# Kernel optimization log

Hardware: AMD Instinct MI355X
Metric: run time of the kernel (lower is better)

## Reference

```python
import jax, jax.numpy as jnp
import numpy as np
from jax import lax

B, T, D, H, K = 8, 1024, 1024, 16, 3
DK = D // H


def setup_inputs() -> dict:
    key = jax.random.key(0)
    ks = jax.random.split(key, 12)
    s = 0.02
    queries = jax.random.normal(ks[0], (B, T, D), dtype=jnp.float32)
    keys = jax.random.normal(ks[1], (B, T, D), dtype=jnp.float32)
    values = jax.random.normal(ks[2], (B, T, D), dtype=jnp.float32)
    # causal mask: True = masked (strict upper triangle)
    attn_mask = jnp.triu(jnp.ones((T, T), dtype=bool), k=1)
    # key padding mask: last 128 keys padded for every batch element
    src_key_padding_mask = jnp.broadcast_to(jnp.arange(T) >= T - 128, (B, T))
    conv_q_w = jax.random.normal(ks[3], (D, D, K), dtype=jnp.float32) * s  # (out, in, k)
    conv_q_b = jax.random.normal(ks[4], (D,), dtype=jnp.float32) * s
    conv_k_w = jax.random.normal(ks[5], (D, D, K), dtype=jnp.float32) * s
    conv_k_b = jax.random.normal(ks[6], (D,), dtype=jnp.float32) * s
    v_w = jax.random.normal(ks[7], (D, D), dtype=jnp.float32) * s   # torch Linear weight [out,in]
    v_b = jax.random.normal(ks[8], (D,), dtype=jnp.float32) * s
    out_w = jax.random.normal(ks[9], (D, D), dtype=jnp.float32) * s
    out_b = jax.random.normal(ks[10], (D,), dtype=jnp.float32) * s
    return {"queries": queries, "keys": keys, "values": values,
            "attn_mask": attn_mask, "src_key_padding_mask": src_key_padding_mask,
            "conv_q_w": conv_q_w, "conv_q_b": conv_q_b,
            "conv_k_w": conv_k_w, "conv_k_b": conv_k_b,
            "v_w": v_w, "v_b": v_b, "out_w": out_w, "out_b": out_b}


def _conv1d_same(x, w, b):
    # x: [B, T, D] -> conv over time with 'same' padding (pad_l=(K-1)//2, pad_r=K//2)
    pad_l, pad_r = (K - 1) // 2, K // 2
    xc = jnp.pad(x.transpose(0, 2, 1), ((0, 0), (0, 0), (pad_l, pad_r)))  # [B, D, T+K-1]
    y = lax.conv_general_dilated(xc, w, window_strides=(1,), padding='VALID',
                                 dimension_numbers=('NCH', 'OIH', 'NCH'))  # [B, D, T]
    return y.transpose(0, 2, 1) + b  # [B, T, D]


def _attention(queries, keys, values, attn_mask, key_padding_mask,
               conv_q_w, conv_q_b, conv_k_w, conv_k_b, v_w, v_b, out_w, out_b):
    q_out = _conv1d_same(queries, conv_q_w, conv_q_b)  # [B, Tq, D]
    k_out = _conv1d_same(keys, conv_k_w, conv_k_b)     # [B, Tk, D]
    v_out = values @ v_w.T + v_b                        # [B, Tk, D]

    Q = q_out.reshape(B, T, H, DK).transpose(0, 2, 1, 3)  # [B, H, Tq, dk]
    Kh = k_out.reshape(B, T, H, DK).transpose(0, 2, 1, 3)
    V = v_out.reshape(B, T, H, DK).transpose(0, 2, 1, 3)

    scores = jnp.einsum('bhqd,bhkd->bhqk', Q, Kh) / jnp.sqrt(jnp.float32(DK))
    neg = jnp.float32(-jnp.inf)
    scores = jnp.where(key_padding_mask[:, None, None, :], neg, scores)
    scores = jnp.where(attn_mask[None, None, :, :], neg, scores)
    attn_weights = jax.nn.softmax(scores, axis=-1)  # dropout is identity at eval
    attn_output = jnp.einsum('bhqk,bhkd->bhqd', attn_weights, V)
    attn_output = attn_output.transpose(0, 2, 1, 3).reshape(B, T, D)
    return attn_output @ out_w.T + out_b, attn_weights


def reference(queries, keys, values, attn_mask, src_key_padding_mask,
              conv_q_w, conv_q_b, conv_k_w, conv_k_b, v_w, v_b, out_w, out_b):
    return _attention(queries, keys, values, attn_mask, src_key_padding_mask,
                      conv_q_w, conv_q_b, conv_k_w, conv_k_b, v_w, v_b, out_w, out_b)
```

## Files before the change

kernel.cpp:

```cpp
#include <hip/hip_runtime.h>

typedef unsigned short u16;
typedef unsigned int   u32;
typedef __bf16 bf16x8 __attribute__((ext_vector_type(8)));
typedef float  f32x4  __attribute__((ext_vector_type(4)));
typedef const __attribute__((address_space(1))) u32* gas1_t;
typedef __attribute__((address_space(3))) u32*       las3_t;

#define DEV static __device__ __forceinline__
#define MFMA16(a, b, c) __builtin_amdgcn_mfma_f32_16x16x32_bf16((a), (b), (c), 0, 0, 0)

DEV u16 f2b(float f) {
  u32 u = __builtin_bit_cast(u32, f);
  return (u16)((u + 0x7fffu + ((u >> 16) & 1u)) >> 16);
}
DEV float b2f(u16 h) { return __builtin_bit_cast(float, (u32)h << 16); }

DEV void stage16(const void* g, void* l) {
  __builtin_amdgcn_global_load_lds((gas1_t)g, (las3_t)l, 16, 0, 0);
}

DEV int rfl(int x) { return __builtin_amdgcn_readfirstlane(x); }

extern "C" __global__ __launch_bounds__(256)
void k_prep(const float* __restrict__ s0, const float* __restrict__ s1,
            const float* __restrict__ s2, const float* __restrict__ s3,
            const float* __restrict__ s4, const float* __restrict__ wq,
            const float* __restrict__ wk, u16* __restrict__ dqkv,
            u16* __restrict__ dvw, u16* __restrict__ dow,
            u16* __restrict__ wtbase, u16* __restrict__ zbuf) {
  __shared__ float ls[3072];
  const int y = blockIdx.y, tid = threadIdx.x;
  if (y < 5) {
    const float* src = y == 0 ? s0 : y == 1 ? s1 : y == 2 ? s2 : y == 3 ? s3 : s4;
    u16* dst = y < 3 ? dqkv + (size_t)y * 8388608 : (y == 3 ? dvw : dow);
    const int n4 = y < 3 ? 2097152 : 262144;
    int i = blockIdx.x * 256 + tid;
    int st = gridDim.x * 256;
    for (; i < n4; i += st) {
      float4 v = ((const float4*)src)[i];
      ushort4 o;
      o.x = f2b(v.x); o.y = f2b(v.y); o.z = f2b(v.z); o.w = f2b(v.w);
      ((ushort4*)dst)[i] = o;
    }
  } else if (y < 7) {
    const int o = blockIdx.x, zz = y - 5;
    const float* src = (zz ? wk : wq) + (size_t)o * 3072;
#pragma unroll
    for (int s = 0; s < 3; ++s)
      ((float4*)ls)[s * 256 + tid] = ((const float4*)src)[s * 256 + tid];
    __syncthreads();
    u16* dst = wtbase + (size_t)zz * 3145728 + (size_t)o * 3072;
#pragma unroll
    for (int s = 0; s < 12; ++s) {
      int j = s * 256 + tid;
      int k = j >> 10, ii = j & 1023;
      dst[j] = f2b(ls[ii * 3 + k]);
    }
  } else {
    if (blockIdx.x == 0) zbuf[tid] = 0;
  }
}

template <int FUSED3, int OUTF32>
__global__ __launch_bounds__(256)
void k_gemm(const u16* __restrict__ Abase, const u16* __restrict__ Btbase,
            const float* __restrict__ b0, const float* __restrict__ b1,
            const float* __restrict__ b2, void* __restrict__ Cbase,
            u16* __restrict__ vT, const u16* __restrict__ zbuf) {
  __shared__ __align__(16) u16 smem[17408];
  const int z = FUSED3 ? blockIdx.z : 0;
  const bool conv = FUSED3 && (z < 2);
  const int K = conv ? 3072 : 1024;
  const u16* A = Abase + (size_t)z * 8388608;
  const u16* Bt = Btbase + (size_t)z * 3145728;
  const float* bias = z == 0 ? b0 : z == 1 ? b1 : b2;
  const int tid = threadIdx.x, lane = tid & 63, wave = tid >> 6;
  const int wm = wave >> 1, wn = wave & 1;
  const int l15 = lane & 15, gr = lane >> 4;
  const int r0 = blockIdx.y * 128, n0 = blockIdx.x * 128;
  const int srow = tid >> 3, scol = (tid & 7) * 8;
  u16* sA = smem;
  f32x4 acc[4][4] = {};

  if (conv) {
    u16* sB = smem + 8320;
    const int bb = r0 >> 10;
    const int tb = (r0 & 1023) - 1;
#pragma unroll 1
    for (int t = 0; t < 16; ++t) {
      const int c0 = t * 64;
#pragma unroll
      for (int s = 0; s < 5; ++s) {
        const int e = s * 256 + tid;
        if (e < 1040) {
          const int lr = e >> 3, ch = (e & 7) * 8;
          const int tt = tb + lr;
          const u16* g = ((u32)tt < 1024u)
              ? (A + (((size_t)((bb << 10) + tt)) << 10) + c0 + ch)
              : (zbuf + ch);
          stage16(g, (char*)smem + rfl((s * 256 + wave * 64) * 16));
        }
      }
#pragma unroll
      for (int s3 = 0; s3 < 3; ++s3) {
#pragma unroll
        for (int s = 0; s < 4; ++s) {
          const int row = s * 32 + srow;
          stage16(Bt + (size_t)(n0 + row) * 3072 + s3 * 1024 + c0 + scol,
                  (char*)smem + rfl(16640 + (s * 256 + wave * 64) * 16));
        }
        __syncthreads();
#pragma unroll
        for (int ks = 0; ks < 2; ++ks) {
          bf16x8 af[4], bfr[4];
          const int koff = ks * 32 + gr * 8;
#pragma unroll
          for (int f = 0; f < 4; ++f)
            af[f] = *(const bf16x8*)&sA[(wm * 64 + f * 16 + l15 + s3) * 64 + koff];
#pragma unroll
          for (int f = 0; f < 4; ++f)
            bfr[f] = *(const bf16x8*)&sB[(wn * 64 + f * 16 + l15) * 64 + koff];
#pragma unroll
          for (int i = 0; i < 4; ++i)
#pragma unroll
            for (int j = 0; j < 4; ++j)
              acc[i][j] = MFMA16(af[i], bfr[j], acc[i][j]);
        }
        __syncthreads();
      }
    }
  } else {
    u16* sB = smem + 8192;
    const int nt = K >> 6;
    for (int t = 0; t < nt; ++t) {
      const int k0 = t * 64;
#pragma unroll
      for (int s = 0; s < 4; ++s) {
        const int row = s * 32 + srow;
        stage16(A + (size_t)(r0 + row) * K + k0 + scol,
                (char*)smem + rfl((s * 256 + wave * 64) * 16));
        stage16(Bt + (size_t)(n0 + row) * K + k0 + scol,
                (char*)smem + rfl(16384 + (s * 256 + wave * 64) * 16));
      }
      __syncthreads();
#pragma unroll
      for (int ks = 0; ks < 2; ++ks) {
        bf16x8 af[4], bfr[4];
        const int koff = ks * 32 + gr * 8;
#pragma unroll
        for (int f = 0; f < 4; ++f)
          af[f] = *(const bf16x8*)&sA[(wm * 64 + f * 16 + l15) * 64 + koff];
#pragma unroll
        for (int f = 0; f < 4; ++f)
          bfr[f] = *(const bf16x8*)&sB[(wn * 64 + f * 16 + l15) * 64 + koff];
#pragma unroll
        for (int i = 0; i < 4; ++i)
#pragma unroll
          for (int j = 0; j < 4; ++j)
            acc[i][j] = MFMA16(af[i], bfr[j], acc[i][j]);
      }
      __syncthreads();
    }
  }

  if (FUSED3 && z == 2) {
    u16* tp = smem;
#pragma unroll
    for (int i = 0; i < 4; ++i)
#pragma unroll
      for (int j = 0; j < 4; ++j) {
        const int cl = wn * 64 + j * 16 + l15;
        const float bv = bias[n0 + cl];
        const int rl0 = wm * 64 + i * 16 + gr * 4;
        union { u16 h[4]; ushort4 v4; } tv;
#pragma unroll
        for (int r = 0; r < 4; ++r) tv.h[r] = f2b(acc[i][j][r] + bv);
        *(ushort4*)&tp[cl * 136 + rl0] = tv.v4;
      }
    __syncthreads();
    const int bb2 = r0 >> 10, tof = r0 & 1023;
    const int drb = tid >> 4, ch16 = (tid & 15) * 8;
#pragma unroll
    for (int g = 0; g < 8; ++g) {
      const int dr = g * 16 + drb;
      uint4 v4 = *(const uint4*)&tp[dr * 136 + ch16];
      *(uint4*)&vT[(((size_t)((bb2 << 10) + n0 + dr)) << 10) + tof + ch16] = v4;
    }
  } else {
    void* Cout = OUTF32 ? Cbase : (void*)((u16*)Cbase + (size_t)z * 8388608);
#pragma unroll
    for (int i = 0; i < 4; ++i)
#pragma unroll
      for (int j = 0; j < 4; ++j) {
        const int colg = n0 + wn * 64 + j * 16 + l15;
        const float bv = bias[colg];
#pragma unroll
        for (int r = 0; r < 4; ++r) {
          const int rowg = r0 + wm * 64 + i * 16 + gr * 4 + r;
          float v = acc[i][j][r] + bv;
          if (OUTF32) ((float*)Cout)[(size_t)rowg * 1024 + colg] = v;
          else        ((u16*)Cout)[(size_t)rowg * 1024 + colg] = f2b(v);
        }
      }
  }
}

__global__ __launch_bounds__(256)
void k_attn(const u16* __restrict__ Qg, const u16* __restrict__ Kg,
            const u16* __restrict__ Vtg, float* __restrict__ Wout,
            u16* __restrict__ Og) {
  __shared__ __align__(16) u16 sQ[128 * 64];
  __shared__ __align__(16) u16 sK[64 * 64];
  __shared__ __align__(16) u16 sV[64 * 64];
  __shared__ __align__(16) u16 sP[4][32 * 64];
  const int tid = threadIdx.x, lane = tid & 63, wave = tid >> 6;
  const int q0 = blockIdx.x * 128, h = blockIdx.y, b = blockIdx.z;
  const u16* Qh = Qg + ((size_t)b * 1024) * 1024 + h * 64;
  const u16* Kh = Kg + ((size_t)b * 1024) * 1024 + h * 64;
  const u16* Vh = Vtg + (size_t)b * 1024 * 1024 + ((size_t)h * 64) * 1024;
  float* Wh = Wout + (((size_t)b * 16 + h) * 1024) * 1024;

#pragma unroll
  for (int s = 0; s < 4; ++s) {
    int e = s * 256 + tid;
    int row = e >> 3, col = (e & 7) * 8;
    stage16(Qh + (size_t)(q0 + row) * 1024 + col,
            (char*)sQ + rfl((s * 256 + wave * 64) * 16));
  }
  const int qw0 = q0 + wave * 32;
  const int rmaxw = (qw0 + 31 < 895) ? (qw0 + 31) : 895;
  const int ktw = (rmaxw >> 6) + 1;
  const int rmaxg = (q0 + 127 < 895) ? (q0 + 127) : 895;
  const int ktmax = (rmaxg >> 6) + 1;

  float l[2][4] = {};

  for (int kt = 0; kt < ktmax; ++kt) {
#pragma unroll
    for (int s = 0; s < 2; ++s) {
      int e = s * 256 + tid;
      int row = e >> 3, col = (e & 7) * 8;
      stage16(Kh + (size_t)(kt * 64 + row) * 1024 + col,
              (char*)sK + rfl((s * 256 + wave * 64) * 16));
    }
    __syncthreads();
    if (kt < ktw) {
      f32x4 sc[2][4] = {};
#pragma unroll
      for (int ks = 0; ks < 2; ++ks) {
        bf16x8 af[2], bfr[4];
        const int koff = ks * 32 + (lane >> 4) * 8;
        af[0] = *(const bf16x8*)&sQ[(wave * 32 + (lane & 15)) * 64 + koff];
        af[1] = *(const bf16x8*)&sQ[(wave * 32 + 16 + (lane & 15)) * 64 + koff];
#pragma unroll
        for (int f = 0; f < 4; ++f)
          bfr[f] = *(const bf16x8*)&sK[(f * 16 + (lane & 15)) * 64 + koff];
#pragma unroll
        for (int i = 0; i < 2; ++i)
#pragma unroll
          for (int f = 0; f < 4; ++f) sc[i][f] = MFMA16(af[i], bfr[f], sc[i][f]);
      }
#pragma unroll
      for (int i = 0; i < 2; ++i)
#pragma unroll
        for (int r = 0; r < 4; ++r) {
          const int rowg = qw0 + i * 16 + (lane >> 4) * 4 + r;
          float ss = 0.f;
#pragma unroll
          for (int f = 0; f < 4; ++f) {
            const int colg = kt * 64 + f * 16 + (lane & 15);
            if (colg <= rowg && colg < 896) ss += __expf(sc[i][f][r] * 0.125f);
          }
#pragma unroll
          for (int d = 1; d < 16; d <<= 1) ss += __shfl_xor(ss, d, 16);
          l[i][r] += ss;
        }
    }
    __syncthreads();
  }

  float rl[2][4];
#pragma unroll
  for (int i = 0; i < 2; ++i)
#pragma unroll
    for (int r = 0; r < 4; ++r) rl[i][r] = 1.f / l[i][r];

  for (int r = 0; r < 32; ++r) {
    float* wrow = Wh + (size_t)(qw0 + r) * 1024;
    for (int c = ktw * 64 + lane * 4; c < 1024; c += 256)
      *(float4*)&wrow[c] = make_float4(0.f, 0.f, 0.f, 0.f);
  }

  f32x4 oa[2][4] = {};
  for (int kt = 0; kt < ktmax; ++kt) {
#pragma unroll
    for (int s = 0; s < 2; ++s) {
      int e = s * 256 + tid;
      int row = e >> 3, col = (e & 7) * 8;
      stage16(Kh + (size_t)(kt * 64 + row) * 1024 + col,
              (char*)sK + rfl((s * 256 + wave * 64) * 16));
      stage16(Vh + (size_t)row * 1024 + kt * 64 + col,
              (char*)sV + rfl((s * 256 + wave * 64) * 16));
    }
    __syncthreads();
    if (kt < ktw) {
      f32x4 sc[2][4] = {};
#pragma unroll
      for (int ks = 0; ks < 2; ++ks) {
        bf16x8 af[2], bfr[4];
        const int koff = ks * 32 + (lane >> 4) * 8;
        af[0] = *(const bf16x8*)&sQ[(wave * 32 + (lane & 15)) * 64 + koff];
        af[1] = *(const bf16x8*)&sQ[(wave * 32 + 16 + (lane & 15)) * 64 + koff];
#pragma unroll
        for (int f = 0; f < 4; ++f)
          bfr[f] = *(const bf16x8*)&sK[(f * 16 + (lane & 15)) * 64 + koff];
#pragma unroll
        for (int i = 0; i < 2; ++i)
#pragma unroll
          for (int f = 0; f < 4; ++f) sc[i][f] = MFMA16(af[i], bfr[f], sc[i][f]);
      }
#pragma unroll
      for (int i = 0; i < 2; ++i)
#pragma unroll
        for (int r = 0; r < 4; ++r) {
          const int rowl = i * 16 + (lane >> 4) * 4 + r;
          const int rowg = qw0 + rowl;
#pragma unroll
          for (int f = 0; f < 4; ++f) {
            const int colt = f * 16 + (lane & 15);
            const int colg = kt * 64 + colt;
            float p = (colg <= rowg && colg < 896)
                          ? __expf(sc[i][f][r] * 0.125f) * rl[i][r] : 0.f;
            sP[wave][rowl * 64 + colt] = f2b(p);
          }
        }
      asm volatile("s_waitcnt lgkmcnt(0)" ::: "memory");
#pragma unroll
      for (int ks = 0; ks < 2; ++ks) {
        bf16x8 af[2], bfr[4];
        const int koff = ks * 32 + (lane >> 4) * 8;
        af[0] = *(const bf16x8*)&sP[wave][(lane & 15) * 64 + koff];
        af[1] = *(const bf16x8*)&sP[wave][(16 + (lane & 15)) * 64 + koff];
#pragma unroll
        for (int f = 0; f < 4; ++f)
          bfr[f] = *(const bf16x8*)&sV[(f * 16 + (lane & 15)) * 64 + koff];
#pragma unroll
        for (int i = 0; i < 2; ++i)
#pragma unroll
          for (int f = 0; f < 4; ++f) oa[i][f] = MFMA16(af[i], bfr[f], oa[i][f]);
      }
#pragma unroll
      for (int rr = 0; rr < 8; ++rr) {
        const int rowl = rr * 4 + (lane >> 4);
        const int c4 = (lane & 15) * 4;
        union { u16 h[4]; uint2 v2; } t;
        t.v2 = *(const uint2*)&sP[wave][rowl * 64 + c4];
        float4 o;
        o.x = b2f(t.h[0]); o.y = b2f(t.h[1]); o.z = b2f(t.h[2]); o.w = b2f(t.h[3]);
        *(float4*)&Wh[(size_t)(qw0 + rowl) * 1024 + kt * 64 + c4] = o;
      }
    }
    __syncthreads();
  }
#pragma unroll
  for (int i = 0; i < 2; ++i)
#pragma unroll
    for (int f = 0; f < 4; ++f)
#pragma unroll
      for (int r = 0; r < 4; ++r) {
        const int rowg = qw0 + i * 16 + (lane >> 4) * 4 + r;
        const int dd = f * 16 + (lane & 15);
        Og[((size_t)b * 1024 + rowg) * 1024 + h * 64 + dd] = f2b(oa[i][f][r]);
      }
}

extern "C" void kernel_launch(void* const* d_in, const int* in_sizes, int n_in,
                              void* d_out, int out_size, void* d_ws, size_t ws_size,
                              hipStream_t stream) {
  const float* queries  = (const float*)d_in[0];
  const float* keys     = (const float*)d_in[1];
  const float* values   = (const float*)d_in[2];
  const float* conv_q_w = (const float*)d_in[5];
  const float* conv_q_b = (const float*)d_in[6];
  const float* conv_k_w = (const float*)d_in[7];
  const float* conv_k_b = (const float*)d_in[8];
  const float* v_w      = (const float*)d_in[9];
  const float* v_b      = (const float*)d_in[10];
  const float* out_w    = (const float*)d_in[11];
  const float* out_b    = (const float*)d_in[12];

  float* out0 = (float*)d_out;
  float* outW = out0 + (size_t)8 * 1024 * 1024;

  char* W = (char*)d_ws;
  u16* qkv_bf = (u16*)(W + (size_t)0);
  u16* wt     = (u16*)(W + (size_t)50331648);
  u16* ow_t   = (u16*)(W + (size_t)65011712);
  u16* q_out  = (u16*)(W + (size_t)67108864);
  u16* zbuf   = (u16*)(W + (size_t)117440512);
  u16* vw_t   = wt + (size_t)2 * 3145728;
  u16* k_out  = q_out + (size_t)8388608;
  u16* v_outT = q_out + (size_t)2 * 8388608;
  u16* a_out  = qkv_bf + 8388608;

  dim3 blk(256);
  k_prep<<<dim3(1024, 8), blk, 0, stream>>>(queries, keys, values, v_w, out_w,
                                            conv_q_w, conv_k_w, qkv_bf, vw_t,
                                            ow_t, wt, zbuf);

  k_gemm<1, 0><<<dim3(8, 64, 3), blk, 0, stream>>>(
      qkv_bf, wt, conv_q_b, conv_k_b, v_b, (void*)q_out, v_outT, zbuf);
  k_attn<<<dim3(8, 16, 8), blk, 0, stream>>>(q_out, k_out, v_outT, outW, a_out);
  k_gemm<0, 1><<<dim3(8, 64, 1), blk, 0, stream>>>(
      a_out, ow_t, out_b, out_b, out_b, (void*)out0, v_outT, zbuf);
}
```

Measured before the change: 446.9 us.

## Load attention Q/K/V fragments directly from global, drop shared staging and block barriers

The attention kernel no longer stages Q, K and V tiles into shared memory with block-wide barriers. Each wave now loads its Q fragments into registers once and reads K and V MFMA fragments straight from global memory, looping only to its own causal limit instead of the block maximum. MFMA sections are wrapped in s_setprio to favour matrix issue. This removes __syncthreads stalls and idle waves on causally-empty tiles, at the cost of redundant uncoalesced global/L2 reads across the four waves.

```diff
diff --git a/kernel.cpp b/kernel.cpp
--- a/kernel.cpp
+++ b/kernel.cpp
@@ -210,74 +210,59 @@
 void k_attn(const u16* __restrict__ Qg, const u16* __restrict__ Kg,
             const u16* __restrict__ Vtg, float* __restrict__ Wout,
             u16* __restrict__ Og) {
-  __shared__ __align__(16) u16 sQ[128 * 64];
-  __shared__ __align__(16) u16 sK[64 * 64];
-  __shared__ __align__(16) u16 sV[64 * 64];
   __shared__ __align__(16) u16 sP[4][32 * 64];
   const int tid = threadIdx.x, lane = tid & 63, wave = tid >> 6;
+  const int l15 = lane & 15, gr = lane >> 4;
   const int q0 = blockIdx.x * 128, h = blockIdx.y, b = blockIdx.z;
-  const u16* Qh = Qg + ((size_t)b * 1024) * 1024 + h * 64;
-  const u16* Kh = Kg + ((size_t)b * 1024) * 1024 + h * 64;
-  const u16* Vh = Vtg + (size_t)b * 1024 * 1024 + ((size_t)h * 64) * 1024;
-  float* Wh = Wout + (((size_t)b * 16 + h) * 1024) * 1024;
-
-#pragma unroll
-  for (int s = 0; s < 4; ++s) {
-    int e = s * 256 + tid;
-    int row = e >> 3, col = (e & 7) * 8;
-    stage16(Qh + (size_t)(q0 + row) * 1024 + col,
-            (char*)sQ + rfl((s * 256 + wave * 64) * 16));
-  }
+  const u16* Qh = Qg + ((size_t)b << 20) + h * 64;
+  const u16* Kh = Kg + ((size_t)b << 20) + h * 64;
+  const u16* Vh = Vtg + ((size_t)b << 20) + ((size_t)(h * 64) << 10);
+  float* Wh = Wout + ((size_t)(b * 16 + h) << 20);
   const int qw0 = q0 + wave * 32;
   const int rmaxw = (qw0 + 31 < 895) ? (qw0 + 31) : 895;
   const int ktw = (rmaxw >> 6) + 1;
-  const int rmaxg = (q0 + 127 < 895) ? (q0 + 127) : 895;
-  const int ktmax = (rmaxg >> 6) + 1;
+
+  bf16x8 qf[2][2];
+#pragma unroll
+  for (int i = 0; i < 2; ++i)
+#pragma unroll
+    for (int ks = 0; ks < 2; ++ks)
+      qf[i][ks] = *(const bf16x8*)
+          &Qh[(size_t)(qw0 + i * 16 + l15) * 1024 + ks * 32 + gr * 8];
 
   float l[2][4] = {};
 
-  for (int kt = 0; kt < ktmax; ++kt) {
-#pragma unroll
-    for (int s = 0; s < 2; ++s) {
-      int e = s * 256 + tid;
-      int row = e >> 3, col = (e & 7) * 8;
-      stage16(Kh + (size_t)(kt * 64 + row) * 1024 + col,
-              (char*)sK + rfl((s * 256 + wave * 64) * 16));
-    }
-    __syncthreads();
-    if (kt < ktw) {
-      f32x4 sc[2][4] = {};
-#pragma unroll
-      for (int ks = 0; ks < 2; ++ks) {
-        bf16x8 af[2], bfr[4];
-        const int koff = ks * 32 + (lane >> 4) * 8;
-        af[0] = *(const bf16x8*)&sQ[(wave * 32 + (lane & 15)) * 64 + koff];
-        af[1] = *(const bf16x8*)&sQ[(wave * 32 + 16 + (lane & 15)) * 64 + koff];
-#pragma unroll
-        for (int f = 0; f < 4; ++f)
-          bfr[f] = *(const bf16x8*)&sK[(f * 16 + (lane & 15)) * 64 + koff];
-#pragma unroll
-        for (int i = 0; i < 2; ++i)
-#pragma unroll
-          for (int f = 0; f < 4; ++f) sc[i][f] = MFMA16(af[i], bfr[f], sc[i][f]);
-      }
+  for (int kt = 0; kt < ktw; ++kt) {
+    f32x4 sc[2][4] = {};
+#pragma unroll
+    for (int ks = 0; ks < 2; ++ks) {
+      bf16x8 kf[4];
+#pragma unroll
+      for (int f = 0; f < 4; ++f)
+        kf[f] = *(const bf16x8*)
+            &Kh[(size_t)(kt * 64 + f * 16 + l15) * 1024 + ks * 32 + gr * 8];
+      __builtin_amdgcn_s_setprio(1);
 #pragma unroll
       for (int i = 0; i < 2; ++i)
 #pragma unroll
-        for (int r = 0; r < 4; ++r) {
-          const int rowg = qw0 + i * 16 + (lane >> 4) * 4 + r;
-          float ss = 0.f;
-#pragma unroll
-          for (int f = 0; f < 4; ++f) {
-            const int colg = kt * 64 + f * 16 + (lane & 15);
-            if (colg <= rowg && colg < 896) ss += __expf(sc[i][f][r] * 0.125f);
-          }
-#pragma unroll
-          for (int d = 1; d < 16; d <<= 1) ss += __shfl_xor(ss, d, 16);
-          l[i][r] += ss;
-        }
-    }
-    __syncthreads();
+        for (int f = 0; f < 4; ++f) sc[i][f] = MFMA16(qf[i][ks], kf[f], sc[i][f]);
+      __builtin_amdgcn_s_setprio(0);
+    }
+#pragma unroll
+    for (int i = 0; i < 2; ++i)
+#pragma unroll
+      for (int r = 0; r < 4; ++r) {
+        const int rowg = qw0 + i * 16 + gr * 4 + r;
+        float ss = 0.f;
+#pragma unroll
+        for (int f = 0; f < 4; ++f) {
+          const int colg = kt * 64 + f * 16 + l15;
+          if (colg <= rowg && colg < 896) ss += __expf(sc[i][f][r] * 0.125f);
+        }
+#pragma unroll
+        for (int d = 1; d < 16; d <<= 1) ss += __shfl_xor(ss, d, 16);
+        l[i][r] += ss;
+      }
   }
 
   float rl[2][4];
@@ -293,75 +278,66 @@
   }
 
   f32x4 oa[2][4] = {};
-  for (int kt = 0; kt < ktmax; ++kt) {
-#pragma unroll
-    for (int s = 0; s < 2; ++s) {
-      int e = s * 256 + tid;
-      int row = e >> 3, col = (e & 7) * 8;
-      stage16(Kh + (size_t)(kt * 64 + row) * 1024 + col,
-              (char*)sK + rfl((s * 256 + wave * 64) * 16));
-      stage16(Vh + (size_t)row * 1024 + kt * 64 + col,
-              (char*)sV + rfl((s * 256 + wave * 64) * 16));
-    }
-    __syncthreads();
-    if (kt < ktw) {
-      f32x4 sc[2][4] = {};
-#pragma unroll
-      for (int ks = 0; ks < 2; ++ks) {
-        bf16x8 af[2], bfr[4];
-        const int koff = ks * 32 + (lane >> 4) * 8;
-        af[0] = *(const bf16x8*)&sQ[(wave * 32 + (lane & 15)) * 64 + koff];
-        af[1] = *(const bf16x8*)&sQ[(wave * 32 + 16 + (lane & 15)) * 64 + koff];
-#pragma unroll
-        for (int f = 0; f < 4; ++f)
-          bfr[f] = *(const bf16x8*)&sK[(f * 16 + (lane & 15)) * 64 + koff];
-#pragma unroll
-        for (int i = 0; i < 2; ++i)
-#pragma unroll
-          for (int f = 0; f < 4; ++f) sc[i][f] = MFMA16(af[i], bfr[f], sc[i][f]);
-      }
+  for (int kt = 0; kt < ktw; ++kt) {
+    f32x4 sc[2][4] = {};
+#pragma unroll
+    for (int ks = 0; ks < 2; ++ks) {
+      bf16x8 kf[4];
+#pragma unroll
+      for (int f = 0; f < 4; ++f)
+        kf[f] = *(const bf16x8*)
+            &Kh[(size_t)(kt * 64 + f * 16 + l15) * 1024 + ks * 32 + gr * 8];
+      __builtin_amdgcn_s_setprio(1);
 #pragma unroll
       for (int i = 0; i < 2; ++i)
 #pragma unroll
-        for (int r = 0; r < 4; ++r) {
-          const int rowl = i * 16 + (lane >> 4) * 4 + r;
-          const int rowg = qw0 + rowl;
-#pragma unroll
-          for (int f = 0; f < 4; ++f) {
-            const int colt = f * 16 + (lane & 15);
-            const int colg = kt * 64 + colt;
-            float p = (colg <= rowg && colg < 896)
-                          ? __expf(sc[i][f][r] * 0.125f) * rl[i][r] : 0.f;
-            sP[wave][rowl * 64 + colt] = f2b(p);
-          }
-        }
-      asm volatile("s_waitcnt lgkmcnt(0)" ::: "memory");
-#pragma unroll
-      for (int ks = 0; ks < 2; ++ks) {
-        bf16x8 af[2], bfr[4];
-        const int koff = ks * 32 + (lane >> 4) * 8;
-        af[0] = *(const bf16x8*)&sP[wave][(lane & 15) * 64 + koff];
-        af[1] = *(const bf16x8*)&sP[wave][(16 + (lane & 15)) * 64 + koff];
-#pragma unroll
-        for (int f = 0; f < 4; ++f)
-          bfr[f] = *(const bf16x8*)&sV[(f * 16 + (lane & 15)) * 64 + koff];
-#pragma unroll
-        for (int i = 0; i < 2; ++i)
-#pragma unroll
-          for (int f = 0; f < 4; ++f) oa[i][f] = MFMA16(af[i], bfr[f], oa[i][f]);
-      }
-#pragma unroll
-      for (int rr = 0; rr < 8; ++rr) {
-        const int rowl = rr * 4 + (lane >> 4);
-        const int c4 = (lane & 15) * 4;
-        union { u16 h[4]; uint2 v2; } t;
-        t.v2 = *(const uint2*)&sP[wave][rowl * 64 + c4];
-        float4 o;
-        o.x = b2f(t.h[0]); o.y = b2f(t.h[1]); o.z = b2f(t.h[2]); o.w = b2f(t.h[3]);
-        *(float4*)&Wh[(size_t)(qw0 + rowl) * 1024 + kt * 64 + c4] = o;
-      }
-    }
-    __syncthreads();
+        for (int f = 0; f < 4; ++f) sc[i][f] = MFMA16(qf[i][ks], kf[f], sc[i][f]);
+      __builtin_amdgcn_s_setprio(0);
+    }
+#pragma unroll
+    for (int i = 0; i < 2; ++i)
+#pragma unroll
+      for (int r = 0; r < 4; ++r) {
+        const int rowl = i * 16 + gr * 4 + r;
+        const int rowg = qw0 + rowl;
+#pragma unroll
+        for (int f = 0; f < 4; ++f) {
+          const int colt = f * 16 + l15;
+          const int colg = kt * 64 + colt;
+          float p = (colg <= rowg && colg < 896)
+                        ? __expf(sc[i][f][r] * 0.125f) * rl[i][r] : 0.f;
+          sP[wave][rowl * 64 + colt] = f2b(p);
+        }
+      }
+    asm volatile("s_waitcnt lgkmcnt(0)" ::: "memory");
+#pragma unroll
+    for (int ks = 0; ks < 2; ++ks) {
+      const int koff = ks * 32 + gr * 8;
+      bf16x8 paf[2], vf[4];
+      paf[0] = *(const bf16x8*)&sP[wave][l15 * 64 + koff];
+      paf[1] = *(const bf16x8*)&sP[wave][(16 + l15) * 64 + koff];
+#pragma unroll
+      for (int f = 0; f < 4; ++f)
+        vf[f] = *(const bf16x8*)
+            &Vh[(size_t)(f * 16 + l15) * 1024 + kt * 64 + koff];
+      __builtin_amdgcn_s_setprio(1);
+#pragma unroll
+      for (int i = 0; i < 2; ++i)
+#pragma unroll
+        for (int f = 0; f < 4; ++f) oa[i][f] = MFMA16(paf[i], vf[f], oa[i][f]);
+      __builtin_amdgcn_s_setprio(0);
+    }
+#pragma unroll
+    for (int rr = 0; rr < 8; ++rr) {
+      const int rowl = rr * 4 + gr;
+      const int c4 = l15 * 4;
+      union { u16 h[4]; uint2 v2; } t;
+      t.v2 = *(const uint2*)&sP[wave][rowl * 64 + c4];
+      float4 o;
+      o.x = b2f(t.h[0]); o.y = b2f(t.h[1]); o.z = b2f(t.h[2]); o.w = b2f(t.h[3]);
+      *(float4*)&Wh[(size_t)(qw0 + rowl) * 1024 + kt * 64 + c4] = o;
+    }
+    asm volatile("s_waitcnt lgkmcnt(0)" ::: "memory");
   }
 #pragma unroll
   for (int i = 0; i < 2; ++i)
@@ -369,8 +345,8 @@
     for (int f = 0; f < 4; ++f)
 #pragma unroll
       for (int r = 0; r < 4; ++r) {
-        const int rowg = qw0 + i * 16 + (lane >> 4) * 4 + r;
-        const int dd = f * 16 + (lane & 15);
+        const int rowg = qw0 + i * 16 + gr * 4 + r;
+        const int dd = f * 16 + l15;
         Og[((size_t)b * 1024 + rowg) * 1024 + h * 64 + dd] = f2b(oa[i][f][r]);
       }
 }
```

After: 474.4 us. +6.1%, slower.
